# Optimization experiments

Measured on AMD Instinct MI355X. Metric: run time of the kernel, lower is better.

Reference implementation:

```python
import jax, jax.numpy as jnp
import numpy as np

N_EMBED = 512
E_DIM = 256
BETA = 0.25


def setup_inputs() -> dict:
    key = jax.random.key(0)
    k1, k2 = jax.random.split(key)
    z = jax.random.normal(k1, (32, 16, 16, 16, E_DIM), dtype=jnp.float32)
    embedding = jax.random.normal(k2, (N_EMBED, E_DIM), dtype=jnp.float32)
    return {"z": z, "embedding": embedding}


def reference(z, embedding):
    # Flatten spatial/batch dims: [N, e_dim]
    zf = z.reshape(-1, E_DIM)
    # similarity = ||z||^2 + ||e||^2 - 2 z.e  (squared distances)
    sim = (
        jnp.sum(zf * zf, axis=1, keepdims=True)
        + jnp.sum(embedding * embedding, axis=1)
        - 2.0 * jnp.einsum("bd,nd->bn", zf, embedding)
    )
    # NOTE: original code uses argmax (farthest code) -- faithfully reproduced.
    codebook_idxs = jnp.argmax(sim, axis=-1)
    # histogram side-effect: codebook_hist[idx] += 1
    hist = jnp.zeros((N_EMBED,), dtype=jnp.float32).at[codebook_idxs].add(1.0)
    z_q = embedding[codebook_idxs].reshape(z.shape)
    vq_loss = jnp.mean((z_q - jax.lax.stop_gradient(z)) ** 2)
    commitment_loss = BETA * jnp.mean((jax.lax.stop_gradient(z_q) - z) ** 2)
    # straight-through estimator
    z_q_st = z + jax.lax.stop_gradient(z_q - z)
    return (z_q_st, vq_loss, commitment_loss, codebook_idxs, hist)
```

## Files before the change

### kernel.cpp

```cpp
#include <hip/hip_runtime.h>
#include <hip/hip_bf16.h>

#define D 256
#define NC 512
#define NROWS 131072L

#define OFF_ZQ   0L
#define OFF_VQ   33554432L
#define OFF_CM   33554433L
#define OFF_IDX  33554434L
#define OFF_HIST 33685506L

#define WS_LPART 0
#define WS_HIST  2048
#define WS_E2    2560
#define WS_CNT   3072
#define WS_AMB   3136
#define WS_FIDX  134208
#define WS_BK    265280
#define WS_NEED  (330816L * 4)

#define MARGIN 1.25f

typedef __attribute__((ext_vector_type(8))) short bf16x8;
typedef __attribute__((ext_vector_type(4))) float f32x4;

#define AS1 __attribute__((address_space(1)))
#define AS3 __attribute__((address_space(3)))

__device__ __forceinline__ unsigned short f2bf(float f) {
    union { float f; unsigned int u; } a; a.f = f;
    return (unsigned short)((a.u + 0x7FFFu + ((a.u >> 16) & 1u)) >> 16);
}

__global__ void vq_init(float* __restrict__ ws) {
    int i = blockIdx.x * 1024 + threadIdx.x;
    if (i < 3073) ws[i] = 0.0f;
}

__global__ void vq_e2(const float* __restrict__ e, float* __restrict__ e2) {
    int c = blockIdx.x;
    int l = threadIdx.x;
    float4 v = *(const float4*)(e + c * D + l * 4);
    float s = v.x * v.x + v.y * v.y + v.z * v.z + v.w * v.w;
    #pragma unroll
    for (int off = 32; off; off >>= 1) s += __shfl_xor(s, off);
    if (l == 0) e2[c] = s;
}

__global__ void vq_convB(const float* __restrict__ e, unsigned short* __restrict__ Bk,
                         float* __restrict__ e2) {
    __shared__ float r4[4];
    int code = blockIdx.x, k = threadIdx.x;
    float v = e[code * D + k];
    Bk[((k >> 5) * NC + code) * 32 + (k & 31)] = f2bf(v);
    float s = v * v;
    #pragma unroll
    for (int off = 32; off; off >>= 1) s += __shfl_xor(s, off);
    if ((k & 63) == 0) r4[k >> 6] = s;
    __syncthreads();
    if (k == 0) e2[code] = r4[0] + r4[1] + r4[2] + r4[3];
}

__global__ __launch_bounds__(512, 4)
void vq_gemm(const float* __restrict__ z, const unsigned short* __restrict__ Bk,
             const float* __restrict__ e2, int* __restrict__ fidx,
             int* __restrict__ acnt, int* __restrict__ alist) {
    __shared__ __align__(16) unsigned short zh[64 * 264];
    __shared__ float red[64 * 25];

    const int tid = threadIdx.x;
    const int w = tid >> 6, l = tid & 63, q = l >> 4, ln = l & 15;
    const long row0 = (long)blockIdx.x * 64;

    #pragma unroll
    for (int j = 0; j < 8; ++j) {
        int c = j * 512 + tid;
        int row = c >> 6, c4 = (c & 63) * 4;
        float4 av = *(const float4*)(z + (row0 + row) * D + c4);
        *(ushort4*)&zh[row * 264 + c4] =
            make_ushort4(f2bf(av.x), f2bf(av.y), f2bf(av.z), f2bf(av.w));
    }
    __syncthreads();

    const unsigned short* bbase = Bk + ((w * 64 + ln) * 32 + q * 8);
    const unsigned short* abase = &zh[ln * 264 + q * 8];

    f32x4 acc[4][4];
    #pragma unroll
    for (int mt = 0; mt < 4; ++mt)
        #pragma unroll
        for (int nt = 0; nt < 4; ++nt) acc[mt][nt] = (f32x4){0.f, 0.f, 0.f, 0.f};

    #pragma unroll
    for (int s = 0; s < 8; ++s) {
        const unsigned short* bs = bbase + s * (NC * 32);
        bf16x8 bfr[4], af[4];
        #pragma unroll
        for (int nt = 0; nt < 4; ++nt)
            bfr[nt] = *(const bf16x8*)(bs + nt * (16 * 32));
        #pragma unroll
        for (int mt = 0; mt < 4; ++mt)
            af[mt] = *(const bf16x8*)(abase + mt * (16 * 264) + s * 32);
        #pragma unroll
        for (int mt = 0; mt < 4; ++mt)
            #pragma unroll
            for (int nt = 0; nt < 4; ++nt)
                acc[mt][nt] = __builtin_amdgcn_mfma_f32_16x16x32_bf16(af[mt], bfr[nt], acc[mt][nt], 0, 0, 0);
    }

    float e2v[4];
    #pragma unroll
    for (int nt = 0; nt < 4; ++nt) e2v[nt] = e2[w * 64 + nt * 16 + ln];

    #pragma unroll
    for (int mt = 0; mt < 4; ++mt) {
        #pragma unroll
        for (int r = 0; r < 4; ++r) {
            float v1 = -3.0e38f, v2 = -3.0e38f; int i1 = 0;
            #pragma unroll
            for (int nt = 0; nt < 4; ++nt) {
                float v = e2v[nt] - 2.0f * acc[mt][nt][r];
                int c = w * 64 + nt * 16 + ln;
                if (v > v1) { v2 = v1; v1 = v; i1 = c; }
                else if (v > v2) v2 = v;
            }
            #pragma unroll
            for (int off = 1; off < 16; off <<= 1) {
                float ov1 = __shfl_xor(v1, off);
                float ov2 = __shfl_xor(v2, off);
                int   oi1 = __shfl_xor(i1, off);
                if (ov1 > v1 || (ov1 == v1 && oi1 < i1)) {
                    v2 = fmaxf(v1, ov2); v1 = ov1; i1 = oi1;
                } else {
                    v2 = fmaxf(v2, ov1);
                }
            }
            if (ln == 0) {
                int rr = mt * 16 + q * 4 + r;
                red[rr * 25 + w * 3 + 0] = v1;
                red[rr * 25 + w * 3 + 1] = (float)i1;
                red[rr * 25 + w * 3 + 2] = v2;
            }
        }
    }
    __syncthreads();
    if (tid < 64) {
        float v1 = -3.0e38f, v2 = -3.0e38f; int i1 = 0;
        #pragma unroll
        for (int g = 0; g < 8; ++g) {
            float rv1 = red[tid * 25 + g * 3 + 0];
            int   ri  = (int)red[tid * 25 + g * 3 + 1];
            float rv2 = red[tid * 25 + g * 3 + 2];
            if (rv1 > v1) { v2 = fmaxf(v1, rv2); v1 = rv1; i1 = ri; }
            else v2 = fmaxf(v2, rv1);
        }
        fidx[row0 + tid] = i1;
        if (v1 - v2 < MARGIN) {
            int ppos = atomicAdd(acnt, 1);
            alist[ppos] = (int)(row0 + tid);
        }
    }
}

__global__ __launch_bounds__(256, 2)
void vq_refine(const float* __restrict__ z, const float* __restrict__ e,
               const float* __restrict__ e2, const int* __restrict__ acnt,
               const int* __restrict__ alist, int* __restrict__ fidx) {
    __shared__ __align__(16) float z_s[32][D];
    __shared__ __align__(16) float e_s[16][NC + 4];
    __shared__ int rowg[32];
    __shared__ int idx_s[32];
    const int tid = threadIdx.x, lane = tid & 63, w = tid >> 6;
    const int cnt = *acnt;
    for (int g = blockIdx.x; g * 32 < cnt; g += gridDim.x) {
        const int base = g * 32;
        __syncthreads();
        if (tid < 32) rowg[tid] = alist[min(base + tid, cnt - 1)];
        __syncthreads();
        #pragma unroll
        for (int j = 0; j < 8; ++j) {
            int c = j * 256 + tid, rl = c >> 6, c4 = (c & 63) * 4;
            *(float4*)&z_s[rl][c4] = *(const float4*)(z + (long)rowg[rl] * D + c4);
        }
        float acc[8][8];
        #pragma unroll
        for (int r = 0; r < 8; ++r)
            #pragma unroll
            for (int c = 0; c < 8; ++c) acc[r][c] = 0.0f;
        const int r0 = w * 8, c_lo = lane * 4;
        for (int kc = 0; kc < D; kc += 16) {
            __syncthreads();
            #pragma unroll
            for (int p = 0; p < 8; ++p) {
                int c = p * 64 + (tid >> 2), kk4 = (tid & 3) * 4;
                float4 v = *(const float4*)(e + c * D + kc + kk4);
                e_s[kk4 + 0][c] = v.x; e_s[kk4 + 1][c] = v.y;
                e_s[kk4 + 2][c] = v.z; e_s[kk4 + 3][c] = v.w;
            }
            __syncthreads();
            #pragma unroll
            for (int k4 = 0; k4 < 16; k4 += 4) {
                float zr[8][4];
                #pragma unroll
                for (int r = 0; r < 8; ++r) *(float4*)zr[r] = *(const float4*)&z_s[r0 + r][kc + k4];
                #pragma unroll
                for (int kk = 0; kk < 4; ++kk) {
                    float ev[8];
                    *(float4*)&ev[0] = *(const float4*)&e_s[k4 + kk][c_lo];
                    *(float4*)&ev[4] = *(const float4*)&e_s[k4 + kk][c_lo + 256];
                    #pragma unroll
                    for (int r = 0; r < 8; ++r)
                        #pragma unroll
                        for (int c = 0; c < 8; ++c) acc[r][c] = fmaf(zr[r][kk], ev[c], acc[r][c]);
                }
            }
        }
        float e2v[8];
        #pragma unroll
        for (int gg = 0; gg < 2; ++gg)
            #pragma unroll
            for (int i = 0; i < 4; ++i) e2v[gg * 4 + i] = e2[gg * 256 + c_lo + i];
        #pragma unroll
        for (int r = 0; r < 8; ++r) {
            float bvv = -3.0e38f; int bc = 0;
            #pragma unroll
            for (int c = 0; c < 8; ++c) {
                int col = (c >> 2) * 256 + c_lo + (c & 3);
                float v = e2v[c] - 2.0f * acc[r][c];
                if (v > bvv) { bvv = v; bc = col; }
            }
            #pragma unroll
            for (int off = 32; off; off >>= 1) {
                float ov = __shfl_xor(bvv, off); int oc = __shfl_xor(bc, off);
                if (ov > bvv || (ov == bvv && oc < bc)) { bvv = ov; bc = oc; }
            }
            if (lane == 0) idx_s[r0 + r] = bc;
        }
        __syncthreads();
        if (tid < 32 && base + tid < cnt) fidx[rowg[tid]] = idx_s[tid];
    }
}

__global__ __launch_bounds__(256)
void vq_hist(const int* __restrict__ fidx, float* __restrict__ out,
             float* __restrict__ hist) {
    __shared__ int h[NC];
    const int t = threadIdx.x;
    h[t] = 0; h[t + 256] = 0;
    __syncthreads();
    const long base = (long)blockIdx.x * 2048;
    #pragma unroll
    for (int j = 0; j < 8; ++j) {
        long i = base + j * 256 + t;
        int idx = fidx[i];
        out[OFF_IDX + i] = (float)idx;
        atomicAdd(&h[idx], 1);
    }
    __syncthreads();
    #pragma unroll
    for (int j = 0; j < 2; ++j) {
        int k = j * 256 + t;
        int c = h[k];
        if (c) atomicAdd(&hist[k], (float)c);
    }
}

__global__ __launch_bounds__(256)
void vq_epi(const float* __restrict__ z, const float* __restrict__ e,
            const int* __restrict__ fidx, float* __restrict__ out,
            float* __restrict__ lpart) {
    __shared__ int idxs[64];
    __shared__ float rs[4];
    const int t = threadIdx.x, lane = t & 63, w = t >> 6;
    const long row0 = (long)blockIdx.x * 64;
    if (t < 64) idxs[t] = fidx[row0 + t];
    __syncthreads();
    float ls = 0.f;
    #pragma unroll 4
    for (int j = 0; j < 16; ++j) {
        const int r = w * 16 + j;
        const long row = row0 + r;
        const int idx = idxs[r];
        float4 zv = *(const float4*)(z + row * D + lane * 4);
        float4 ev = *(const float4*)(e + (long)idx * D + lane * 4);
        float4 dq;
        dq.x = ev.x - zv.x; dq.y = ev.y - zv.y; dq.z = ev.z - zv.z; dq.w = ev.w - zv.w;
        float4 o;
        o.x = zv.x + dq.x; o.y = zv.y + dq.y; o.z = zv.z + dq.z; o.w = zv.w + dq.w;
        *(float4*)(out + OFF_ZQ + row * D + lane * 4) = o;
        ls += dq.x * dq.x + dq.y * dq.y + dq.z * dq.z + dq.w * dq.w;
    }
    #pragma unroll
    for (int off = 32; off; off >>= 1) ls += __shfl_xor(ls, off);
    if (lane == 0) rs[w] = ls;
    __syncthreads();
    if (t == 0) lpart[blockIdx.x] = rs[0] + rs[1] + rs[2] + rs[3];
}

__global__ void vq_fin(const float* __restrict__ ws, float* __restrict__ out) {
    __shared__ float sred[16];
    const int t = threadIdx.x, lane = t & 63, w = t >> 6;
    float s = ws[WS_LPART + t] + ws[WS_LPART + t + 1024];
    #pragma unroll
    for (int off = 32; off; off >>= 1) s += __shfl_xor(s, off);
    if (lane == 0) sred[w] = s;
    __syncthreads();
    if (t == 0) {
        float tot = 0.f;
        #pragma unroll
        for (int i = 0; i < 16; ++i) tot += sred[i];
        float m = tot / 33554432.0f;
        out[OFF_VQ] = m;
        out[OFF_CM] = 0.25f * m;
    }
    if (t < NC) out[OFF_HIST + t] = ws[WS_HIST + t];
}

__global__ __launch_bounds__(256, 2)
void vq_main_fb(const float* __restrict__ z, const float* __restrict__ e,
                const float* __restrict__ e2, float* __restrict__ out,
                float* __restrict__ ws_loss, float* __restrict__ ws_hist) {
    __shared__ __align__(16) float z_s[32][D];
    __shared__ __align__(16) float e_s[16][NC + 4];
    __shared__ int   idx_s[32];
    __shared__ float red_s[4];
    const int tid = threadIdx.x, lane = tid & 63, w = tid >> 6;
    const long row0 = (long)blockIdx.x * 32;
    {
        const float4* zg = (const float4*)(z + row0 * D);
        float4* zs = (float4*)(&z_s[0][0]);
        #pragma unroll
        for (int i = 0; i < 8; ++i) zs[i * 256 + tid] = zg[i * 256 + tid];
    }
    float acc[8][8];
    #pragma unroll
    for (int r = 0; r < 8; ++r)
        #pragma unroll
        for (int c = 0; c < 8; ++c) acc[r][c] = 0.0f;
    const int r0 = w * 8, c_lo = lane * 4;
    for (int kc = 0; kc < D; kc += 16) {
        __syncthreads();
        #pragma unroll
        for (int p = 0; p < 8; ++p) {
            int c = p * 64 + (tid >> 2), kk4 = (tid & 3) * 4;
            float4 v = *(const float4*)(e + c * D + kc + kk4);
            e_s[kk4 + 0][c] = v.x; e_s[kk4 + 1][c] = v.y;
            e_s[kk4 + 2][c] = v.z; e_s[kk4 + 3][c] = v.w;
        }
        __syncthreads();
        #pragma unroll
        for (int k4 = 0; k4 < 16; k4 += 4) {
            float zr[8][4];
            #pragma unroll
            for (int r = 0; r < 8; ++r) *(float4*)zr[r] = *(const float4*)&z_s[r0 + r][kc + k4];
            #pragma unroll
            for (int kk = 0; kk < 4; ++kk) {
                float ev[8];
                *(float4*)&ev[0] = *(const float4*)&e_s[k4 + kk][c_lo];
                *(float4*)&ev[4] = *(const float4*)&e_s[k4 + kk][c_lo + 256];
                #pragma unroll
                for (int r = 0; r < 8; ++r)
                    #pragma unroll
                    for (int c = 0; c < 8; ++c) acc[r][c] = fmaf(zr[r][kk], ev[c], acc[r][c]);
            }
        }
    }
    float e2v[8];
    #pragma unroll
    for (int g = 0; g < 2; ++g)
        #pragma unroll
        for (int i = 0; i < 4; ++i) e2v[g * 4 + i] = e2[g * 256 + c_lo + i];
    #pragma unroll
    for (int r = 0; r < 8; ++r) {
        float bvv = -3.0e38f; int bc = 0;
        #pragma unroll
        for (int c = 0; c < 8; ++c) {
            int col = (c >> 2) * 256 + c_lo + (c & 3);
            float v = e2v[c] - 2.0f * acc[r][c];
            if (v > bvv) { bvv = v; bc = col; }
        }
        #pragma unroll
        for (int off = 32; off; off >>= 1) {
            float ov = __shfl_xor(bvv, off); int oc = __shfl_xor(bc, off);
            if (ov > bvv || (ov == bvv && oc < bc)) { bvv = ov; bc = oc; }
        }
        if (lane == 0) idx_s[r0 + r] = bc;
    }
    __syncthreads();
    if (tid < 32) {
        int bc = idx_s[tid];
        out[OFF_IDX + row0 + tid] = (float)bc;
        atomicAdd(&ws_hist[bc], 1.0f);
    }
    float lsum = 0.0f;
    for (int r = 0; r < 32; ++r) {
        int idx = idx_s[r];
        float ev = e[idx * D + tid];
        float zv = z_s[r][tid];
        float dq = ev - zv;
        out[OFF_ZQ + (row0 + r) * D + tid] = zv + dq;
        lsum += dq * dq;
    }
    #pragma unroll
    for (int off = 32; off; off >>= 1) lsum += __shfl_xor(lsum, off);
    if (lane == 0) red_s[w] = lsum;
    __syncthreads();
    if (tid == 0) atomicAdd(ws_loss, red_s[0] + red_s[1] + red_s[2] + red_s[3]);
}

__global__ void vq_init_fb(float* __restrict__ ws) {
    int t = threadIdx.x;
    if (t < 513) ws[t] = 0.0f;
}
__global__ void vq_fin_fb(const float* __restrict__ ws, float* __restrict__ out) {
    int t = blockIdx.x * blockDim.x + threadIdx.x;
    if (t < NC) out[OFF_HIST + t] = ws[1 + t];
    if (t == NC) {
        float m = ws[0] / 33554432.0f;
        out[OFF_VQ] = m; out[OFF_CM] = 0.25f * m;
    }
}

extern "C" void kernel_launch(void* const* d_in, const int* in_sizes, int n_in,
                              void* d_out, int out_size, void* d_ws, size_t ws_size,
                              hipStream_t stream) {
    const float* z = (const float*)d_in[0];
    const float* e = (const float*)d_in[1];
    float* out = (float*)d_out;
    float* ws  = (float*)d_ws;

    if (ws_size >= (size_t)WS_NEED) {
        float* lpart = ws + WS_LPART;
        float* hist  = ws + WS_HIST;
        float* e2    = ws + WS_E2;
        int*   acnt  = (int*)(ws + WS_CNT);
        int*   alist = (int*)(ws + WS_AMB);
        int*   fidx  = (int*)(ws + WS_FIDX);
        unsigned short* Bk = (unsigned short*)(ws + WS_BK);

        vq_init<<<4, 1024, 0, stream>>>(ws);
        vq_convB<<<NC, 256, 0, stream>>>(e, Bk, e2);
        vq_gemm<<<2048, 512, 0, stream>>>(z, Bk, e2, fidx, acnt, alist);
        vq_refine<<<512, 256, 0, stream>>>(z, e, e2, acnt, alist, fidx);
        vq_hist<<<64, 256, 0, stream>>>(fidx, out, hist);
        vq_epi<<<2048, 256, 0, stream>>>(z, e, fidx, out, lpart);
        vq_fin<<<1, 1024, 0, stream>>>(ws, out);
    } else {
        float* ws_loss = ws;
        float* ws_hist = ws + 1;
        float* ws_e2   = ws + 513;
        vq_init_fb<<<1, 1024, 0, stream>>>(ws);
        vq_e2<<<NC, 64, 0, stream>>>(e, ws_e2);
        vq_main_fb<<<4096, 256, 0, stream>>>(z, e, ws_e2, out, ws_loss, ws_hist);
        vq_fin_fb<<<3, 256, 0, stream>>>(ws, out);
    }
}
```

Before: 402.5 us.

## Prefetch B fragments, simplify argmax reduction, aggregate atomics, fold init kernel

```diff
diff --git a/kernel.cpp b/kernel.cpp
--- a/kernel.cpp
+++ b/kernel.cpp
@@ -33,11 +33,6 @@
     return (unsigned short)((a.u + 0x7FFFu + ((a.u >> 16) & 1u)) >> 16);
 }
 
-__global__ void vq_init(float* __restrict__ ws) {
-    int i = blockIdx.x * 1024 + threadIdx.x;
-    if (i < 3073) ws[i] = 0.0f;
-}
-
 __global__ void vq_e2(const float* __restrict__ e, float* __restrict__ e2) {
     int c = blockIdx.x;
     int l = threadIdx.x;
@@ -49,7 +44,8 @@
 }
 
 __global__ void vq_convB(const float* __restrict__ e, unsigned short* __restrict__ Bk,
-                         float* __restrict__ e2) {
+                         float* __restrict__ e2, float* __restrict__ hist,
+                         int* __restrict__ acnt) {
     __shared__ float r4[4];
     int code = blockIdx.x, k = threadIdx.x;
     float v = e[code * D + k];
@@ -58,11 +54,15 @@
     #pragma unroll
     for (int off = 32; off; off >>= 1) s += __shfl_xor(s, off);
     if ((k & 63) == 0) r4[k >> 6] = s;
+    if (k == 0) {
+        hist[code] = 0.0f;
+        if (code == 0) *acnt = 0;
+    }
     __syncthreads();
     if (k == 0) e2[code] = r4[0] + r4[1] + r4[2] + r4[3];
 }
 
-__global__ __launch_bounds__(512, 4)
+__global__ __launch_bounds__(512, 3)
 void vq_gemm(const float* __restrict__ z, const unsigned short* __restrict__ Bk,
              const float* __restrict__ e2, int* __restrict__ fidx,
              int* __restrict__ acnt, int* __restrict__ alist) {
@@ -72,6 +72,12 @@
     const int tid = threadIdx.x;
     const int w = tid >> 6, l = tid & 63, q = l >> 4, ln = l & 15;
     const long row0 = (long)blockIdx.x * 64;
+
+    const unsigned short* bbase = Bk + ((w * 64 + ln) * 32 + q * 8);
+    bf16x8 bnx[4];
+    #pragma unroll
+    for (int nt = 0; nt < 4; ++nt)
+        bnx[nt] = *(const bf16x8*)(bbase + nt * (16 * 32));
 
     #pragma unroll
     for (int j = 0; j < 8; ++j) {
@@ -83,7 +89,6 @@
     }
     __syncthreads();
 
-    const unsigned short* bbase = Bk + ((w * 64 + ln) * 32 + q * 8);
     const unsigned short* abase = &zh[ln * 264 + q * 8];
 
     f32x4 acc[4][4];
@@ -94,11 +99,15 @@
 
     #pragma unroll
     for (int s = 0; s < 8; ++s) {
-        const unsigned short* bs = bbase + s * (NC * 32);
-        bf16x8 bfr[4], af[4];
-        #pragma unroll
-        for (int nt = 0; nt < 4; ++nt)
-            bfr[nt] = *(const bf16x8*)(bs + nt * (16 * 32));
+        bf16x8 bcur[4], af[4];
+        #pragma unroll
+        for (int nt = 0; nt < 4; ++nt) bcur[nt] = bnx[nt];
+        if (s < 7) {
+            const unsigned short* bs = bbase + (s + 1) * (NC * 32);
+            #pragma unroll
+            for (int nt = 0; nt < 4; ++nt)
+                bnx[nt] = *(const bf16x8*)(bs + nt * (16 * 32));
+        }
         #pragma unroll
         for (int mt = 0; mt < 4; ++mt)
             af[mt] = *(const bf16x8*)(abase + mt * (16 * 264) + s * 32);
@@ -106,7 +115,7 @@
         for (int mt = 0; mt < 4; ++mt)
             #pragma unroll
             for (int nt = 0; nt < 4; ++nt)
-                acc[mt][nt] = __builtin_amdgcn_mfma_f32_16x16x32_bf16(af[mt], bfr[nt], acc[mt][nt], 0, 0, 0);
+                acc[mt][nt] = __builtin_amdgcn_mfma_f32_16x16x32_bf16(af[mt], bcur[nt], acc[mt][nt], 0, 0, 0);
     }
 
     float e2v[4];
@@ -120,22 +129,23 @@
             float v1 = -3.0e38f, v2 = -3.0e38f; int i1 = 0;
             #pragma unroll
             for (int nt = 0; nt < 4; ++nt) {
-                float v = e2v[nt] - 2.0f * acc[mt][nt][r];
+                float v = fmaf(-2.0f, acc[mt][nt][r], e2v[nt]);
                 int c = w * 64 + nt * 16 + ln;
                 if (v > v1) { v2 = v1; v1 = v; i1 = c; }
-                else if (v > v2) v2 = v;
-            }
+                else v2 = fmaxf(v2, v);
+            }
+            float v1p = v1;
             #pragma unroll
             for (int off = 1; off < 16; off <<= 1) {
                 float ov1 = __shfl_xor(v1, off);
                 float ov2 = __shfl_xor(v2, off);
-                int   oi1 = __shfl_xor(i1, off);
-                if (ov1 > v1 || (ov1 == v1 && oi1 < i1)) {
-                    v2 = fmaxf(v1, ov2); v1 = ov1; i1 = oi1;
-                } else {
-                    v2 = fmaxf(v2, ov1);
-                }
-            }
+                v2 = fmaxf(fmaxf(v2, ov2), fminf(v1, ov1));
+                v1 = fmaxf(v1, ov1);
+            }
+            unsigned long long mm = __ballot(v1p == v1);
+            unsigned int gm = (unsigned int)((mm >> (q * 16)) & 0xFFFFULL);
+            int src = q * 16 + (__ffs(gm) - 1);
+            i1 = __shfl(i1, src);
             if (ln == 0) {
                 int rr = mt * 16 + q * 4 + r;
                 red[rr * 25 + w * 3 + 0] = v1;
@@ -156,9 +166,15 @@
             else v2 = fmaxf(v2, rv1);
         }
         fidx[row0 + tid] = i1;
-        if (v1 - v2 < MARGIN) {
-            int ppos = atomicAdd(acnt, 1);
-            alist[ppos] = (int)(row0 + tid);
+        int amb = (v1 - v2 < MARGIN) ? 1 : 0;
+        unsigned long long m = __ballot(amb);
+        int nb = __popcll(m);
+        int basep = 0;
+        if (tid == 0 && nb) basep = atomicAdd(acnt, nb);
+        basep = __shfl(basep, 0);
+        if (amb) {
+            int pfx = __popcll(m & ((1ULL << tid) - 1ULL));
+            alist[basep + pfx] = (int)(row0 + tid);
         }
     }
 }
@@ -243,8 +259,7 @@
 }
 
 __global__ __launch_bounds__(256)
-void vq_hist(const int* __restrict__ fidx, float* __restrict__ out,
-             float* __restrict__ hist) {
+void vq_hist(const int* __restrict__ fidx, float* __restrict__ hist) {
     __shared__ int h[NC];
     const int t = threadIdx.x;
     h[t] = 0; h[t + 256] = 0;
@@ -253,9 +268,7 @@
     #pragma unroll
     for (int j = 0; j < 8; ++j) {
         long i = base + j * 256 + t;
-        int idx = fidx[i];
-        out[OFF_IDX + i] = (float)idx;
-        atomicAdd(&h[idx], 1);
+        atomicAdd(&h[fidx[i]], 1);
     }
     __syncthreads();
     #pragma unroll
@@ -274,7 +287,11 @@
     __shared__ float rs[4];
     const int t = threadIdx.x, lane = t & 63, w = t >> 6;
     const long row0 = (long)blockIdx.x * 64;
-    if (t < 64) idxs[t] = fidx[row0 + t];
+    if (t < 64) {
+        int ix = fidx[row0 + t];
+        idxs[t] = ix;
+        out[OFF_IDX + row0 + t] = (float)ix;
+    }
     __syncthreads();
     float ls = 0.f;
     #pragma unroll 4
@@ -385,7 +402,7 @@
             float ov = __shfl_xor(bvv, off); int oc = __shfl_xor(bc, off);
             if (ov > bvv || (ov == bvv && oc < bc)) { bvv = ov; bc = oc; }
         }
-        if (lane == 0) idx_s[r0 + r] = bc;
+        if (lane == 0) idx_s[r] = bc;
     }
     __syncthreads();
     if (tid < 32) {
@@ -439,11 +456,10 @@
         int*   fidx  = (int*)(ws + WS_FIDX);
         unsigned short* Bk = (unsigned short*)(ws + WS_BK);
 
-        vq_init<<<4, 1024, 0, stream>>>(ws);
-        vq_convB<<<NC, 256, 0, stream>>>(e, Bk, e2);
+        vq_convB<<<NC, 256, 0, stream>>>(e, Bk, e2, hist, acnt);
         vq_gemm<<<2048, 512, 0, stream>>>(z, Bk, e2, fidx, acnt, alist);
         vq_refine<<<512, 256, 0, stream>>>(z, e, e2, acnt, alist, fidx);
-        vq_hist<<<64, 256, 0, stream>>>(fidx, out, hist);
+        vq_hist<<<64, 256, 0, stream>>>(fidx, hist);
         vq_epi<<<2048, 256, 0, stream>>>(z, e, fidx, out, lpart);
         vq_fin<<<1, 1024, 0, stream>>>(ws, out);
     } else {
```

Measured after the change: 395.3 us. No clear change (-1.8%).
